# Kernel optimization log

Hardware: AMD Instinct MI355X
Metric: run time of the kernel (lower is better)

The kernel has to match this reference:

```python
import jax, jax.numpy as jnp
import numpy as np

B, F_IN, N_D, N_A, VBS, N_STEPS = 1024, 256, 64, 64, 128, 3
FO = N_D + N_A            # 128
D_CAT = 2 * F_IN          # 512
AD = F_IN                 # attention_dim = 256
GAMMA, EPSILON, BN_EPS = 1.3, 1e-15, 1e-5
SQRT_HALF = 0.7071067811865476


def _bn(x, w, b):
    # full-batch BatchNorm1d (training mode, biased var)
    m = x.mean(0)
    v = x.var(0)
    return (x - m) / jnp.sqrt(v + BN_EPS) * w + b


def _gbn(x, w, b):
    # Ghost BatchNorm: per virtual-batch statistics
    n, f = x.shape
    xr = x.reshape(n // VBS, VBS, f)
    m = xr.mean(1, keepdims=True)
    v = xr.var(1, keepdims=True)
    return (xr - m).reshape(n, f) / jnp.sqrt(v + BN_EPS).repeat(VBS, axis=0).reshape(n, f) * w + b


def _glu(x, fcw, bnw, bnb):
    h = _gbn(x @ fcw.T, bnw, bnb)
    d = h.shape[-1] // 2
    return h[:, :d] * jax.nn.sigmoid(h[:, d:])


def _feat_transformer(x, fc0, bnw0, bnb0, fc1, bnw1, bnb1):
    # independent GLU block, first=True, n_glu_independent=2
    h = _glu(x, fc0, bnw0, bnb0)
    return (h + _glu(h, fc1, bnw1, bnb1)) * SQRT_HALF


def _sparsemax(z):
    f = z.shape[-1]
    zs = -jnp.sort(-z, axis=-1)                      # descending
    k = jnp.arange(1, f + 1, dtype=z.dtype)
    zc = jnp.cumsum(zs, axis=-1)
    support = (1.0 + k * zs) > zc
    kz = jnp.sum(support, axis=-1, keepdims=True)
    tau = (jnp.take_along_axis(zc, kz - 1, axis=-1) - 1.0) / kz.astype(z.dtype)
    return jnp.maximum(z - tau, 0.0)


def _self_attn_1d(x, in_w, in_b, out_w, out_b):
    # nn.MultiheadAttention(embed_dim=1, heads=1) over the feature axis
    q = x * in_w[0] + in_b[0]
    k = x * in_w[1] + in_b[1]
    v = x * in_w[2] + in_b[2]
    attn = jax.nn.softmax(jnp.einsum('bi,bj->bij', q, k), axis=-1)  # scale 1/sqrt(1)
    y = jnp.einsum('bij,bj->bi', attn, v) * out_w + out_b
    return y, attn


def setup_inputs() -> dict:
    key = jax.random.key(0)
    ks = iter(jax.random.split(key, 32))
    s = 0.1
    d = {
        'x': jax.random.normal(next(ks), (B, F_IN), jnp.float32),
        'bemv': jax.random.normal(next(ks), (B, F_IN), jnp.float32),
        'gmat': jax.random.uniform(next(ks), (AD, F_IN), jnp.float32),
        'bn_w': jnp.ones((F_IN,), jnp.float32),
        'bn_b': jnp.zeros((F_IN,), jnp.float32),
        'init_fc0': jax.random.normal(next(ks), (2 * FO, D_CAT), jnp.float32) * s,
        'init_bnw0': jnp.ones((2 * FO,), jnp.float32),
        'init_bnb0': jnp.zeros((2 * FO,), jnp.float32),
        'init_fc1': jax.random.normal(next(ks), (2 * FO, FO), jnp.float32) * s,
        'init_bnw1': jnp.ones((2 * FO,), jnp.float32),
        'init_bnb1': jnp.zeros((2 * FO,), jnp.float32),
        'step_fc0': jax.random.normal(next(ks), (N_STEPS, 2 * FO, D_CAT), jnp.float32) * s,
        'step_bnw0': jnp.ones((N_STEPS, 2 * FO), jnp.float32),
        'step_bnb0': jnp.zeros((N_STEPS, 2 * FO), jnp.float32),
        'step_fc1': jax.random.normal(next(ks), (N_STEPS, 2 * FO, FO), jnp.float32) * s,
        'step_bnw1': jnp.ones((N_STEPS, 2 * FO), jnp.float32),
        'step_bnb1': jnp.zeros((N_STEPS, 2 * FO), jnp.float32),
        'att_fc': jax.random.normal(next(ks), (N_STEPS, AD, N_A), jnp.float32) * s,
        'att_bnw': jnp.ones((N_STEPS, AD), jnp.float32),
        'att_bnb': jnp.zeros((N_STEPS, AD), jnp.float32),
        'sa_in_w': jax.random.normal(next(ks), (N_STEPS, 3), jnp.float32),
        'sa_in_b': jnp.zeros((N_STEPS, 3), jnp.float32),
        'sa_out_w': jax.random.normal(next(ks), (N_STEPS,), jnp.float32),
        'sa_out_b': jnp.zeros((N_STEPS,), jnp.float32),
    }
    return d


def reference(x, bemv, gmat, bn_w, bn_b,
              init_fc0, init_bnw0, init_bnb0, init_fc1, init_bnw1, init_bnb1,
              step_fc0, step_bnw0, step_bnb0, step_fc1, step_bnw1, step_bnb1,
              att_fc, att_bnw, att_bnb,
              sa_in_w, sa_in_b, sa_out_w, sa_out_b):
    prior = jnp.ones((x.shape[0], AD), x.dtype)
    xn = _bn(x, bn_w, bn_b)
    x_cat = jnp.concatenate([xn, bemv], axis=1)
    feat_out = _feat_transformer(x_cat, init_fc0, init_bnw0, init_bnb0,
                                 init_fc1, init_bnw1, init_bnb1)
    att = feat_out[:, N_D:]
    m_loss = jnp.asarray(0.0, x.dtype)
    steps, amaps = [], []
    for s in range(N_STEPS):
        a = _gbn(att @ att_fc[s].T, att_bnw[s], att_bnb[s])
        tab_mask = _sparsemax(a * prior)
        m_loss = m_loss + jnp.mean(jnp.sum(tab_mask * jnp.log(tab_mask + EPSILON), axis=1))
        prior = prior * (GAMMA - tab_mask)
        x_masked = (tab_mask @ gmat) * xn
        x_masked, A = _self_attn_1d(x_masked, sa_in_w[s], sa_in_b[s], sa_out_w[s], sa_out_b[s])
        amaps.append(A)
        feat_out = _feat_transformer(jnp.concatenate([x_masked, bemv], axis=1),
                                     step_fc0[s], step_bnw0[s], step_bnb0[s],
                                     step_fc1[s], step_bnw1[s], step_bnb1[s])
        steps.append(jax.nn.leaky_relu(feat_out[:, :N_D], 0.01))
        att = feat_out[:, N_D:]
    m_loss = m_loss / N_STEPS
    return jnp.stack(steps), m_loss, jnp.stack(amaps)
```

## Files before the change

kernel.cpp:

```cpp
#include <hip/hip_runtime.h>
#include <hip/hip_bf16.h>

#define BATCH 1024
#define F_IN 256
#define N_D 64
#define N_A 64
#define VBS 128
#define N_STEPS 3
#define FO 128
#define D_CAT 512
#define AD 256
#define GAMMA_C 1.3f
#define BN_EPS_C 1e-5f
#define SQRT_HALF_C 0.70710678118654752440f

__device__ __forceinline__ float ldin(const void* p, size_t i, int isbf){
  if (isbf) return __bfloat162float(((const __hip_bfloat16*)p)[i]);
  return ((const float*)p)[i];
}
__device__ __forceinline__ float4 ld4(const void* p, size_t i, int isbf){
  if (!isbf) return *(const float4*)((const float*)p + i);
  const __hip_bfloat16* q = (const __hip_bfloat16*)p + i;
  return make_float4(__bfloat162float(q[0]), __bfloat162float(q[1]),
                     __bfloat162float(q[2]), __bfloat162float(q[3]));
}

__device__ __forceinline__ float wsum(float v){
#pragma unroll
  for (int o = 32; o > 0; o >>= 1) v += __shfl_xor(v, o);
  return v;
}
__device__ __forceinline__ float wmaxr(float v){
#pragma unroll
  for (int o = 32; o > 0; o >>= 1) v = fmaxf(v, __shfl_xor(v, o));
  return v;
}
__device__ __forceinline__ float wminr(float v){
#pragma unroll
  for (int o = 32; o > 0; o >>= 1) v = fminf(v, __shfl_xor(v, o));
  return v;
}
__device__ __forceinline__ float block_sum(float v, float* sb){
  int t = threadIdx.x;
  sb[t] = v; __syncthreads();
#pragma unroll
  for (int s = 128; s > 0; s >>= 1){
    if (t < s) sb[t] += sb[t + s];
    __syncthreads();
  }
  float r = sb[0]; __syncthreads();
  return r;
}

__global__ void detect_k(const unsigned short* __restrict__ u, float* __restrict__ flag){
  __shared__ int cnt;
  if (threadIdx.x == 0) cnt = 0;
  __syncthreads();
  int c = 0;
  for (int j = 0; j < 16; ++j){
    unsigned short v = u[(size_t)(threadIdx.x * 16 + j) * 2];
    int e = (v >> 7) & 0xFF;
    if (e >= 118 && e <= 134) c++;
  }
  atomicAdd(&cnt, c);
  __syncthreads();
  if (threadIdx.x == 0) flag[0] = (cnt > 2048) ? 1.0f : 0.0f;
}

__global__ void bnstats_k(const void* __restrict__ x, float* __restrict__ mean,
                          float* __restrict__ istd, const float* __restrict__ flg){
  __shared__ float sb[256];
  const int isbf = flg[0] != 0.0f;
  int f = blockIdx.x, t = threadIdx.x;
  float s = 0.f, ss = 0.f;
  for (int r = t; r < BATCH; r += 256){
    float v = ldin(x, (size_t)r * F_IN + f, isbf);
    s += v; ss += v * v;
  }
  s  = block_sum(s, sb);
  ss = block_sum(ss, sb);
  if (t == 0){
    float m = s * (1.f / BATCH);
    mean[f] = m;
    istd[f] = rsqrtf(ss * (1.f / BATCH) - m * m + BN_EPS_C);
  }
}

__global__ void xn_k(const void* __restrict__ x, const float* __restrict__ mean,
                     const float* __restrict__ istd, const void* __restrict__ bw,
                     const void* __restrict__ bb, float* __restrict__ xn,
                     const float* __restrict__ flg){
  const int isbf = flg[0] != 0.0f;
  int idx = blockIdx.x * 256 + threadIdx.x;
  int f = idx & (F_IN - 1);
  xn[idx] = (ldin(x, idx, isbf) - mean[f]) * istd[f] * ldin(bw, f, isbf) + ldin(bb, f, isbf);
}

__global__ __launch_bounds__(256)
void gemm_bt_k(const float* __restrict__ A1, const void* __restrict__ A2, int split,
               const void* __restrict__ W, size_t woff, float* __restrict__ C,
               int K, const float* __restrict__ flg){
  __shared__ float As[32][34];
  __shared__ float Ws[32][34];
  const int isbf = flg[0] != 0.0f;
  const int n0 = blockIdx.x * 32, m0 = blockIdx.y * 32;
  const int t = threadIdx.x;
  const int tx = t & 15, ty = t >> 4;
  const int lr = t >> 3, lk = (t & 7) * 4;
  const int nc = K >> 5;
  float a00 = 0.f, a01 = 0.f, a10 = 0.f, a11 = 0.f;

  auto lda = [&](int k0) -> float4 {
    int gk = k0 + lk, gr = m0 + lr;
    if (gk < split) return *(const float4*)(A1 + (size_t)gr * split + gk);
    return ld4(A2, (size_t)gr * (K - split) + (gk - split), isbf);
  };
  auto ldw = [&](int k0) -> float4 {
    return ld4(W, woff + (size_t)(n0 + lr) * K + k0 + lk, isbf);
  };

  float4 ra = lda(0), rw = ldw(0);
  for (int c = 0; c < nc; ++c){
    As[lk+0][lr] = ra.x; As[lk+1][lr] = ra.y; As[lk+2][lr] = ra.z; As[lk+3][lr] = ra.w;
    Ws[lk+0][lr] = rw.x; Ws[lk+1][lr] = rw.y; Ws[lk+2][lr] = rw.z; Ws[lk+3][lr] = rw.w;
    __syncthreads();
    float4 na = ra, nw = rw;
    if (c + 1 < nc){ na = lda((c+1) << 5); nw = ldw((c+1) << 5); }
#pragma unroll
    for (int kk = 0; kk < 32; ++kk){
      float2 av = *(const float2*)&As[kk][ty*2];
      float2 wv = *(const float2*)&Ws[kk][tx*2];
      a00 += av.x * wv.x; a01 += av.x * wv.y;
      a10 += av.y * wv.x; a11 += av.y * wv.y;
    }
    __syncthreads();
    ra = na; rw = nw;
  }
  int r0 = m0 + ty*2, c0 = n0 + tx*2;
  float* Cp = C + (size_t)r0 * 256 + c0;
  Cp[0] = a00; Cp[1] = a01; Cp[256] = a10; Cp[257] = a11;
}

__global__ __launch_bounds__(256)
void gemm_glu_k(const float* __restrict__ H1, const float* __restrict__ saf,
                const float* __restrict__ sbf, const void* __restrict__ W,
                size_t woff, float* __restrict__ C, const float* __restrict__ flg){
  __shared__ float As[32][34];
  __shared__ float Ws[32][34];
  const int isbf = flg[0] != 0.0f;
  const int n0 = blockIdx.x * 32, m0 = blockIdx.y * 32;
  const int t = threadIdx.x;
  const int tx = t & 15, ty = t >> 4;
  const int lr = t >> 3, lk = (t & 7) * 4;
  float a00 = 0.f, a01 = 0.f, a10 = 0.f, a11 = 0.f;

  auto lda = [&](int k0) -> float4 {
    int gk = k0 + lk, gr = m0 + lr, g = gr >> 7;
    float4 h0 = *(const float4*)(H1 + (size_t)gr*256 + gk);
    float4 h1 = *(const float4*)(H1 + (size_t)gr*256 + gk + 128);
    float4 A0 = *(const float4*)(saf + g*256 + gk);
    float4 B0 = *(const float4*)(sbf + g*256 + gk);
    float4 A1 = *(const float4*)(saf + g*256 + gk + 128);
    float4 B1 = *(const float4*)(sbf + g*256 + gk + 128);
    float4 r;
    r.x = (h0.x*A0.x + B0.x) / (1.f + __expf(-(h1.x*A1.x + B1.x)));
    r.y = (h0.y*A0.y + B0.y) / (1.f + __expf(-(h1.y*A1.y + B1.y)));
    r.z = (h0.z*A0.z + B0.z) / (1.f + __expf(-(h1.z*A1.z + B1.z)));
    r.w = (h0.w*A0.w + B0.w) / (1.f + __expf(-(h1.w*A1.w + B1.w)));
    return r;
  };
  auto ldw = [&](int k0) -> float4 {
    return ld4(W, woff + (size_t)(n0 + lr) * 128 + k0 + lk, isbf);
  };

  float4 ra = lda(0), rw = ldw(0);
#pragma unroll 1
  for (int c = 0; c < 4; ++c){
    As[lk+0][lr] = ra.x; As[lk+1][lr] = ra.y; As[lk+2][lr] = ra.z; As[lk+3][lr] = ra.w;
    Ws[lk+0][lr] = rw.x; Ws[lk+1][lr] = rw.y; Ws[lk+2][lr] = rw.z; Ws[lk+3][lr] = rw.w;
    __syncthreads();
    float4 na = ra, nw = rw;
    if (c + 1 < 4){ na = lda((c+1) << 5); nw = ldw((c+1) << 5); }
#pragma unroll
    for (int kk = 0; kk < 32; ++kk){
      float2 av = *(const float2*)&As[kk][ty*2];
      float2 wv = *(const float2*)&Ws[kk][tx*2];
      a00 += av.x * wv.x; a01 += av.x * wv.y;
      a10 += av.y * wv.x; a11 += av.y * wv.y;
    }
    __syncthreads();
    ra = na; rw = nw;
  }
  int r0 = m0 + ty*2, c0 = n0 + tx*2;
  float* Cp = C + (size_t)r0 * 256 + c0;
  Cp[0] = a00; Cp[1] = a01; Cp[256] = a10; Cp[257] = a11;
}

__global__ __launch_bounds__(256)
void gstats_k(const float* __restrict__ H, const void* __restrict__ w,
              const void* __restrict__ b, size_t off, float* __restrict__ sa,
              float* __restrict__ sb, const float* __restrict__ flg){
  __shared__ float ps[8][32], pss[8][32];
  const int isbf = flg[0] != 0.0f;
  int c0 = blockIdx.x * 32, g = blockIdx.y;
  int tx = threadIdx.x & 31, q = threadIdx.x >> 5;
  const float* Hp = H + ((size_t)g*128 + q*16) * 256 + c0 + tx;
  float s = 0.f, ss = 0.f;
#pragma unroll
  for (int i = 0; i < 16; ++i){ float v = Hp[(size_t)i*256]; s += v; ss += v*v; }
  ps[q][tx] = s; pss[q][tx] = ss;
  __syncthreads();
  if (threadIdx.x < 32){
    int t = threadIdx.x, col = c0 + t;
    float S = 0.f, SS = 0.f;
#pragma unroll
    for (int qq = 0; qq < 8; ++qq){ S += ps[qq][t]; SS += pss[qq][t]; }
    float m = S * (1.f/128), is = rsqrtf(SS * (1.f/128) - m*m + BN_EPS_C);
    float wv = ldin(w, off + col, isbf), bv = ldin(b, off + col, isbf);
    float A = is * wv;
    sa[g*256 + col] = A;
    sb[g*256 + col] = bv - m * A;
  }
}

__global__ __launch_bounds__(256)
void spmaxxm_k(const float* __restrict__ H, const float* __restrict__ sa,
               const float* __restrict__ sb, float* __restrict__ prior,
               const float* __restrict__ xn, const void* __restrict__ gmat,
               float* __restrict__ xm, float* __restrict__ lrow,
               int first, const float* __restrict__ flg){
  __shared__ __align__(16) float tabs[4][256];
  __shared__ unsigned int msk[4][2];
  const int isbf = flg[0] != 0.0f;
  int lane = threadIdx.x & 63, wv = threadIdx.x >> 6;
  int b0 = blockIdx.x * 4;
  int b = b0 + wv, g = b >> 7;
  size_t rb = (size_t)b * 256;
  int j0 = lane * 4;
  float4 h4 = *(const float4*)(H + rb + j0);
  float4 A4 = *(const float4*)(sa + (size_t)g*256 + j0);
  float4 B4 = *(const float4*)(sb + (size_t)g*256 + j0);
  float pr[4];
  if (first){ pr[0] = pr[1] = pr[2] = pr[3] = 1.f; }
  else { float4 p4 = *(const float4*)(prior + rb + j0); pr[0]=p4.x; pr[1]=p4.y; pr[2]=p4.z; pr[3]=p4.w; }
  float z[4];
  z[0] = (h4.x*A4.x + B4.x) * pr[0];
  z[1] = (h4.y*A4.y + B4.y) * pr[1];
  z[2] = (h4.z*A4.z + B4.z) * pr[2];
  z[3] = (h4.w*A4.w + B4.w) * pr[3];
  float zm = wmaxr(fmaxf(fmaxf(z[0], z[1]), fmaxf(z[2], z[3])));
  float lo = zm - 1.f, hi = zm;
#pragma unroll 1
  for (int it = 0; it < 30; ++it){
    float mid = 0.5f * (lo + hi);
    float s = 0.f;
#pragma unroll
    for (int e = 0; e < 4; ++e){ float d = z[e] - mid; s += d > 0.f ? d : 0.f; }
    s = wsum(s);
    if (s >= 1.f) lo = mid; else hi = mid;
  }
  float tau = 0.5f * (lo + hi);
  float p[4], ls = 0.f;
#pragma unroll
  for (int e = 0; e < 4; ++e){
    p[e] = z[e] - tau; p[e] = p[e] > 0.f ? p[e] : 0.f;
    ls += p[e] * __logf(p[e] + 1e-15f);
  }
  *(float4*)&tabs[wv][j0] = make_float4(p[0], p[1], p[2], p[3]);
  *(float4*)(prior + rb + j0) = make_float4(pr[0]*(GAMMA_C - p[0]), pr[1]*(GAMMA_C - p[1]),
                                            pr[2]*(GAMMA_C - p[2]), pr[3]*(GAMMA_C - p[3]));
  ls = wsum(ls);
  if (lane == 0) lrow[b] = ls;
  bool nz = (p[0] > 0.f) | (p[1] > 0.f) | (p[2] > 0.f) | (p[3] > 0.f);
  unsigned long long bm = __ballot(nz);
  if (lane == 0){ msk[wv][0] = (unsigned int)bm; msk[wv][1] = (unsigned int)(bm >> 32); }
  __syncthreads();
  int t = threadIdx.x;
  unsigned long long M0 = msk[0][0] | ((unsigned long long)msk[0][1] << 32);
  unsigned long long M1 = msk[1][0] | ((unsigned long long)msk[1][1] << 32);
  unsigned long long M2 = msk[2][0] | ((unsigned long long)msk[2][1] << 32);
  unsigned long long M3 = msk[3][0] | ((unsigned long long)msk[3][1] << 32);
  float a0 = 0.f, a1 = 0.f, a2 = 0.f, a3 = 0.f;
#pragma unroll 1
  for (int c = 0; c < 64; ++c){
    int r0a = (int)((M0 >> c) & 1), r1a = (int)((M1 >> c) & 1);
    int r2a = (int)((M2 >> c) & 1), r3a = (int)((M3 >> c) & 1);
    if (r0a | r1a | r2a | r3a){
      int k = c * 4;
      float g0 = ldin(gmat, (size_t)(k+0)*256 + t, isbf);
      float g1 = ldin(gmat, (size_t)(k+1)*256 + t, isbf);
      float g2 = ldin(gmat, (size_t)(k+2)*256 + t, isbf);
      float g3 = ldin(gmat, (size_t)(k+3)*256 + t, isbf);
      if (r0a){ float4 tv = *(float4*)&tabs[0][k]; a0 += tv.x*g0 + tv.y*g1 + tv.z*g2 + tv.w*g3; }
      if (r1a){ float4 tv = *(float4*)&tabs[1][k]; a1 += tv.x*g0 + tv.y*g1 + tv.z*g2 + tv.w*g3; }
      if (r2a){ float4 tv = *(float4*)&tabs[2][k]; a2 += tv.x*g0 + tv.y*g1 + tv.z*g2 + tv.w*g3; }
      if (r3a){ float4 tv = *(float4*)&tabs[3][k]; a3 += tv.x*g0 + tv.y*g1 + tv.z*g2 + tv.w*g3; }
    }
  }
  xm[(size_t)(b0+0)*256 + t] = a0 * xn[(size_t)(b0+0)*256 + t];
  xm[(size_t)(b0+1)*256 + t] = a1 * xn[(size_t)(b0+1)*256 + t];
  xm[(size_t)(b0+2)*256 + t] = a2 * xn[(size_t)(b0+2)*256 + t];
  xm[(size_t)(b0+3)*256 + t] = a3 * xn[(size_t)(b0+3)*256 + t];
}

__global__ __launch_bounds__(256)
void attn_k(const float* __restrict__ xm, float* __restrict__ y,
            const void* __restrict__ in_w, const void* __restrict__ in_b,
            const void* __restrict__ out_w, const void* __restrict__ out_b,
            int s, float* __restrict__ amap, const float* __restrict__ flg){
  __shared__ __align__(16) float qs[256], ks[256], vs[256], ms[256], rz[256];
  __shared__ float r1[4], r2[4];
  const int isbf = flg[0] != 0.0f;
  int b = blockIdx.x, t = threadIdx.x;
  float w0 = ldin(in_w, s*3+0, isbf), w1 = ldin(in_w, s*3+1, isbf), w2 = ldin(in_w, s*3+2, isbf);
  float b0 = ldin(in_b, s*3+0, isbf), b1 = ldin(in_b, s*3+1, isbf), b2 = ldin(in_b, s*3+2, isbf);
  float ow = ldin(out_w, s, isbf), ob = ldin(out_b, s, isbf);
  float xv = xm[(size_t)b*256 + t];
  float q = xv*w0 + b0, k = xv*w1 + b1, v = xv*w2 + b2;
  qs[t] = q; ks[t] = k; vs[t] = v;
  int lane = t & 63, wv = t >> 6;
  float km = wmaxr(k), kn = wminr(k);
  if (lane == 0){ r1[wv] = km; r2[wv] = kn; }
  __syncthreads();
  float kmax = fmaxf(fmaxf(r1[0], r1[1]), fmaxf(r1[2], r1[3]));
  float kmin = fminf(fminf(r2[0], r2[1]), fminf(r2[2], r2[3]));
  float mi = (q >= 0.f) ? q*kmax : q*kmin;
  float Z = 0.f, Y = 0.f;
#pragma unroll 8
  for (int j = 0; j < 256; j += 4){
    float4 k4 = *(const float4*)&ks[j];
    float4 v4 = *(const float4*)&vs[j];
    float e0 = __expf(q*k4.x - mi), e1 = __expf(q*k4.y - mi);
    float e2 = __expf(q*k4.z - mi), e3 = __expf(q*k4.w - mi);
    Z += (e0 + e1) + (e2 + e3);
    Y += (e0*v4.x + e1*v4.y) + (e2*v4.z + e3*v4.w);
  }
  float rzv = 1.f / Z;
  y[(size_t)b*256 + t] = Y*rzv*ow + ob;
  ms[t] = mi; rz[t] = rzv;
  __syncthreads();
  int c0 = (t & 127) * 2;
  int rh = (t >> 7) * 128;
  float k0 = ks[c0], k1 = ks[c0 + 1];
  size_t base = ((size_t)s*BATCH + b) * 65536 + c0;
#pragma unroll 8
  for (int i = 0; i < 128; i += 4){
    int r = rh + i;
    float4 q4 = *(const float4*)&qs[r];
    float4 m4 = *(const float4*)&ms[r];
    float4 s4 = *(const float4*)&rz[r];
    float e00 = __expf(q4.x*k0 - m4.x) * s4.x, e01 = __expf(q4.x*k1 - m4.x) * s4.x;
    float e10 = __expf(q4.y*k0 - m4.y) * s4.y, e11 = __expf(q4.y*k1 - m4.y) * s4.y;
    float e20 = __expf(q4.z*k0 - m4.z) * s4.z, e21 = __expf(q4.z*k1 - m4.z) * s4.z;
    float e30 = __expf(q4.w*k0 - m4.w) * s4.w, e31 = __expf(q4.w*k1 - m4.w) * s4.w;
    *(float2*)(amap + base + (size_t)(r+0)*256) = make_float2(e00, e01);
    *(float2*)(amap + base + (size_t)(r+1)*256) = make_float2(e10, e11);
    *(float2*)(amap + base + (size_t)(r+2)*256) = make_float2(e20, e21);
    *(float2*)(amap + base + (size_t)(r+3)*256) = make_float2(e30, e31);
  }
}

__global__ __launch_bounds__(256)
void combine_k(const float* __restrict__ H1, const float* __restrict__ sa0,
               const float* __restrict__ sb0, const float* __restrict__ H2,
               const float* __restrict__ sa1, const float* __restrict__ sb1,
               float* __restrict__ att, float* __restrict__ steps_out){
  int r = blockIdx.x * 2 + (threadIdx.x >> 7);
  int j = threadIdx.x & 127;
  int g = r >> 7;
  float h0 = H1[(size_t)r*256 + j],  h1 = H1[(size_t)r*256 + j + 128];
  float n0 = h0 * sa0[g*256 + j]     + sb0[g*256 + j];
  float n1 = h1 * sa0[g*256 + j+128] + sb0[g*256 + j+128];
  float g0 = n0 / (1.f + __expf(-n1));
  float h2 = H2[(size_t)r*256 + j],  h3 = H2[(size_t)r*256 + j + 128];
  float m0 = h2 * sa1[g*256 + j]     + sb1[g*256 + j];
  float m1 = h3 * sa1[g*256 + j+128] + sb1[g*256 + j+128];
  float g1 = m0 / (1.f + __expf(-m1));
  float f = (g0 + g1) * SQRT_HALF_C;
  if (j < 64){
    if (steps_out) steps_out[(size_t)r*64 + j] = f > 0.f ? f : 0.01f*f;
  } else {
    att[(size_t)r*64 + (j - 64)] = f;
  }
}

__global__ void mloss_k(const float* __restrict__ lrow, float* __restrict__ outp){
  __shared__ float sb[256];
  int t = threadIdx.x;
  float s = 0.f;
  for (int i = t; i < N_STEPS*BATCH; i += 256) s += lrow[i];
  s = block_sum(s, sb);
  if (t == 0) outp[0] = s * (1.f/(N_STEPS*(float)BATCH));
}

extern "C" void kernel_launch(void* const* d_in, const int* in_sizes, int n_in,
                              void* d_out, int out_size, void* d_ws, size_t ws_size,
                              hipStream_t stream){
  const void* x         = d_in[0];
  const void* bemv      = d_in[1];
  const void* gmat      = d_in[2];
  const void* bn_w      = d_in[3];
  const void* bn_b      = d_in[4];
  const void* init_fc0  = d_in[5];
  const void* init_bnw0 = d_in[6];
  const void* init_bnb0 = d_in[7];
  const void* init_fc1  = d_in[8];
  const void* init_bnw1 = d_in[9];
  const void* init_bnb1 = d_in[10];
  const void* step_fc0  = d_in[11];
  const void* step_bnw0 = d_in[12];
  const void* step_bnb0 = d_in[13];
  const void* step_fc1  = d_in[14];
  const void* step_bnw1 = d_in[15];
  const void* step_bnb1 = d_in[16];
  const void* att_fc    = d_in[17];
  const void* att_bnw   = d_in[18];
  const void* att_bnb   = d_in[19];
  const void* sa_in_w   = d_in[20];
  const void* sa_in_b   = d_in[21];
  const void* sa_out_w  = d_in[22];
  const void* sa_out_b  = d_in[23];

  float* out       = (float*)d_out;
  float* steps_out = out;
  float* mloss_out = out + (size_t)N_STEPS*BATCH*N_D;
  float* amaps     = mloss_out + 1;

  float* w     = (float*)d_ws;
  float* flag  = w;
  float* mean  = w + 16;
  float* istd  = w + 272;
  float* lrow  = w + 528;
  float* sa0   = w + 4096;
  float* sb0   = sa0 + 2048;
  float* sa1   = sb0 + 2048;
  float* sb1   = sa1 + 2048;
  float* saA   = sb1 + 2048;
  float* sbA   = saA + 2048;
  float* xn    = w + 16384;
  float* H1    = xn   + 262144;
  float* H2    = H1   + 262144;
  float* att   = H2   + 262144;
  float* xm    = att  + 65536;
  float* prior = xm   + 262144;
  float* y     = prior + 262144;

  dim3 gemmGrid(8, 32);
  dim3 gstGrid(8, 8);

  detect_k<<<1, 256, 0, stream>>>((const unsigned short*)x, flag);
  bnstats_k<<<256, 256, 0, stream>>>(x, mean, istd, flag);
  xn_k<<<1024, 256, 0, stream>>>(x, mean, istd, bn_w, bn_b, xn, flag);

  gemm_bt_k<<<gemmGrid, 256, 0, stream>>>(xn, bemv, 256, init_fc0, 0, H1, 512, flag);
  gstats_k<<<gstGrid, 256, 0, stream>>>(H1, init_bnw0, init_bnb0, 0, sa0, sb0, flag);
  gemm_glu_k<<<gemmGrid, 256, 0, stream>>>(H1, sa0, sb0, init_fc1, 0, H2, flag);
  gstats_k<<<gstGrid, 256, 0, stream>>>(H2, init_bnw1, init_bnb1, 0, sa1, sb1, flag);
  combine_k<<<512, 256, 0, stream>>>(H1, sa0, sb0, H2, sa1, sb1, att, nullptr);

  for (int s = 0; s < N_STEPS; ++s){
    gemm_bt_k<<<gemmGrid, 256, 0, stream>>>(att, nullptr, 64, att_fc, (size_t)s*AD*N_A, H1, 64, flag);
    gstats_k<<<gstGrid, 256, 0, stream>>>(H1, att_bnw, att_bnb, (size_t)s*256, saA, sbA, flag);
    spmaxxm_k<<<256, 256, 0, stream>>>(H1, saA, sbA, prior, xn, gmat, xm, lrow + s*1024, s == 0, flag);
    attn_k<<<1024, 256, 0, stream>>>(xm, y, sa_in_w, sa_in_b, sa_out_w, sa_out_b, s, amaps, flag);
    gemm_bt_k<<<gemmGrid, 256, 0, stream>>>(y, bemv, 256, step_fc0, (size_t)s*256*512, H1, 512, flag);
    gstats_k<<<gstGrid, 256, 0, stream>>>(H1, step_bnw0, step_bnb0, (size_t)s*256, sa0, sb0, flag);
    gemm_glu_k<<<gemmGrid, 256, 0, stream>>>(H1, sa0, sb0, step_fc1, (size_t)s*256*128, H2, flag);
    gstats_k<<<gstGrid, 256, 0, stream>>>(H2, step_bnw1, step_bnb1, (size_t)s*256, sa1, sb1, flag);
    combine_k<<<512, 256, 0, stream>>>(H1, sa0, sb0, H2, sa1, sb1, att,
                                       steps_out + (size_t)s*BATCH*N_D);
  }
  mloss_k<<<1, 256, 0, stream>>>(lrow, mloss_out);
}
```

Measured before the change: 440.4 us.

## Defer attention-map writes into spare blocks of later kernels; fuse GBN stats into consumers

The attention kernel now stores only per-row q, k, max and 1/Z to a staging buffer instead of writing the full 256x256 attention map per row. Extra "drain" blocks are appended to later kernels (the GEMMs, GLU-GEMM, combine, sparsemax and the next step's attention), and they expand those rows into the amap output. This overlaps the large amap store traffic with compute-bound kernels. Separately, the ghost-batchnorm stats kernels are removed and each consumer block recomputes the group statistics itself. That cuts launches but adds redundant column reductions and a staging buffer round trip.

Result: no change. 443.0 us (+0.6%).

```diff
diff --git a/kernel.cpp b/kernel.cpp
--- a/kernel.cpp
+++ b/kernel.cpp
@@ -2,17 +2,11 @@
 #include <hip/hip_bf16.h>
 
 #define BATCH 1024
-#define F_IN 256
-#define N_D 64
-#define N_A 64
-#define VBS 128
 #define N_STEPS 3
-#define FO 128
-#define D_CAT 512
-#define AD 256
 #define GAMMA_C 1.3f
 #define BN_EPS_C 1e-5f
 #define SQRT_HALF_C 0.70710678118654752440f
+#define ST_STRIDE 786432
 
 __device__ __forceinline__ float ldin(const void* p, size_t i, int isbf){
   if (isbf) return __bfloat162float(((const __hip_bfloat16*)p)[i]);
@@ -52,6 +46,39 @@
   return r;
 }
 
+__device__ __forceinline__ void drain_rows(const float* __restrict__ st,
+                                           float* __restrict__ amap,
+                                           int s, int b, int t){
+  __shared__ __align__(16) float sh[768];
+  const float* qS = st;
+  const float* kS = st + ST_STRIDE;
+  const float* mS = st + 2*ST_STRIDE;
+  const float* rS = st + 3*ST_STRIDE;
+  size_t sb = ((size_t)s*BATCH + b)*256;
+  sh[t]       = qS[sb + t];
+  sh[256 + t] = mS[sb + t];
+  sh[512 + t] = rS[sb + t];
+  __syncthreads();
+  int c0 = (t & 127)*2, rh = (t >> 7)*128;
+  float k0 = kS[sb + c0], k1 = kS[sb + c0 + 1];
+  size_t base = ((size_t)s*BATCH + b)*65536 + c0;
+#pragma unroll 8
+  for (int i = 0; i < 128; i += 4){
+    int r = rh + i;
+    float4 q4 = *(const float4*)&sh[r];
+    float4 m4 = *(const float4*)&sh[256 + r];
+    float4 s4 = *(const float4*)&sh[512 + r];
+    float e00 = __expf(q4.x*k0 - m4.x) * s4.x, e01 = __expf(q4.x*k1 - m4.x) * s4.x;
+    float e10 = __expf(q4.y*k0 - m4.y) * s4.y, e11 = __expf(q4.y*k1 - m4.y) * s4.y;
+    float e20 = __expf(q4.z*k0 - m4.z) * s4.z, e21 = __expf(q4.z*k1 - m4.z) * s4.z;
+    float e30 = __expf(q4.w*k0 - m4.w) * s4.w, e31 = __expf(q4.w*k1 - m4.w) * s4.w;
+    *(float2*)(amap + base + (size_t)(r+0)*256) = make_float2(e00, e01);
+    *(float2*)(amap + base + (size_t)(r+1)*256) = make_float2(e10, e11);
+    *(float2*)(amap + base + (size_t)(r+2)*256) = make_float2(e20, e21);
+    *(float2*)(amap + base + (size_t)(r+3)*256) = make_float2(e30, e31);
+  }
+}
+
 __global__ void detect_k(const unsigned short* __restrict__ u, float* __restrict__ flag){
   __shared__ int cnt;
   if (threadIdx.x == 0) cnt = 0;
@@ -74,7 +101,7 @@
   int f = blockIdx.x, t = threadIdx.x;
   float s = 0.f, ss = 0.f;
   for (int r = t; r < BATCH; r += 256){
-    float v = ldin(x, (size_t)r * F_IN + f, isbf);
+    float v = ldin(x, (size_t)r * 256 + f, isbf);
     s += v; ss += v * v;
   }
   s  = block_sum(s, sb);
@@ -92,19 +119,21 @@
                      const float* __restrict__ flg){
   const int isbf = flg[0] != 0.0f;
   int idx = blockIdx.x * 256 + threadIdx.x;
-  int f = idx & (F_IN - 1);
+  int f = idx & 255;
   xn[idx] = (ldin(x, idx, isbf) - mean[f]) * istd[f] * ldin(bw, f, isbf) + ldin(bb, f, isbf);
 }
 
 __global__ __launch_bounds__(256)
 void gemm_bt_k(const float* __restrict__ A1, const void* __restrict__ A2, int split,
-               const void* __restrict__ W, size_t woff, float* __restrict__ C,
-               int K, const float* __restrict__ flg){
+               const void* __restrict__ W, size_t woff, float* __restrict__ C, int K,
+               const float* __restrict__ st, float* __restrict__ amap, int dS, int dR0,
+               const float* __restrict__ flg){
+  int bid = blockIdx.x, t = threadIdx.x;
+  if (bid >= 256){ drain_rows(st, amap, dS, dR0 + bid - 256, t); return; }
   __shared__ float As[32][34];
   __shared__ float Ws[32][34];
   const int isbf = flg[0] != 0.0f;
-  const int n0 = blockIdx.x * 32, m0 = blockIdx.y * 32;
-  const int t = threadIdx.x;
+  const int n0 = (bid & 7) * 32, m0 = (bid >> 3) * 32;
   const int tx = t & 15, ty = t >> 4;
   const int lr = t >> 3, lk = (t & 7) * 4;
   const int nc = K >> 5;
@@ -142,31 +171,48 @@
 }
 
 __global__ __launch_bounds__(256)
-void gemm_glu_k(const float* __restrict__ H1, const float* __restrict__ saf,
-                const float* __restrict__ sbf, const void* __restrict__ W,
-                size_t woff, float* __restrict__ C, const float* __restrict__ flg){
+void glugemm_k(const float* __restrict__ H1, const void* __restrict__ gw,
+               const void* __restrict__ gb, size_t goff,
+               const void* __restrict__ W, size_t woff, float* __restrict__ C,
+               const float* __restrict__ st, float* __restrict__ amap, int dS, int dR0,
+               const float* __restrict__ flg){
+  int bid = blockIdx.x, t = threadIdx.x;
+  if (bid >= 256){ drain_rows(st, amap, dS, dR0 + bid - 256, t); return; }
+  __shared__ __align__(16) float sA[256], sB[256];
   __shared__ float As[32][34];
   __shared__ float Ws[32][34];
   const int isbf = flg[0] != 0.0f;
-  const int n0 = blockIdx.x * 32, m0 = blockIdx.y * 32;
-  const int t = threadIdx.x;
+  const int n0 = (bid & 7) * 32, m0 = (bid >> 3) * 32;
+  const int g = bid >> 5;
+  {
+    const float* Hp = H1 + (size_t)g*32768 + t;
+    float s = 0.f, ss = 0.f;
+#pragma unroll 8
+    for (int i = 0; i < 128; ++i){ float v = Hp[(size_t)i*256]; s += v; ss += v*v; }
+    float m = s * (1.f/128), is = rsqrtf(ss * (1.f/128) - m*m + BN_EPS_C);
+    float wv = ldin(gw, goff + t, isbf), bv = ldin(gb, goff + t, isbf);
+    float A = is * wv;
+    sA[t] = A; sB[t] = bv - m*A;
+  }
+  __syncthreads();
   const int tx = t & 15, ty = t >> 4;
   const int lr = t >> 3, lk = (t & 7) * 4;
   float a00 = 0.f, a01 = 0.f, a10 = 0.f, a11 = 0.f;
 
   auto lda = [&](int k0) -> float4 {
-    int gk = k0 + lk, gr = m0 + lr, g = gr >> 7;
-    float4 h0 = *(const float4*)(H1 + (size_t)gr*256 + gk);
-    float4 h1 = *(const float4*)(H1 + (size_t)gr*256 + gk + 128);
-    float4 A0 = *(const float4*)(saf + g*256 + gk);
-    float4 B0 = *(const float4*)(sbf + g*256 + gk);
-    float4 A1 = *(const float4*)(saf + g*256 + gk + 128);
-    float4 B1 = *(const float4*)(sbf + g*256 + gk + 128);
+    int gk = k0 + lk, gr = m0 + lr;
+    const float* h = H1 + (size_t)gr*256;
+    float4 h0 = *(const float4*)(h + gk);
+    float4 h1 = *(const float4*)(h + gk + 128);
+    float4 A0 = *(const float4*)(sA + gk);
+    float4 B0 = *(const float4*)(sB + gk);
+    float4 A1 = *(const float4*)(sA + gk + 128);
+    float4 B1 = *(const float4*)(sB + gk + 128);
     float4 r;
-    r.x = (h0.x*A0.x + B0.x) / (1.f + __expf(-(h1.x*A1.x + B1.x)));
-    r.y = (h0.y*A0.y + B0.y) / (1.f + __expf(-(h1.y*A1.y + B1.y)));
-    r.z = (h0.z*A0.z + B0.z) / (1.f + __expf(-(h1.z*A1.z + B1.z)));
-    r.w = (h0.w*A0.w + B0.w) / (1.f + __expf(-(h1.w*A1.w + B1.w)));
+    r.x = (h0.x*A0.x+B0.x) / (1.f + __expf(-(h1.x*A1.x+B1.x)));
+    r.y = (h0.y*A0.y+B0.y) / (1.f + __expf(-(h1.y*A1.y+B1.y)));
+    r.z = (h0.z*A0.z+B0.z) / (1.f + __expf(-(h1.z*A1.z+B1.z)));
+    r.w = (h0.w*A0.w+B0.w) / (1.f + __expf(-(h1.w*A1.w+B1.w)));
     return r;
   };
   auto ldw = [&](int k0) -> float4 {
@@ -197,49 +243,38 @@
 }
 
 __global__ __launch_bounds__(256)
-void gstats_k(const float* __restrict__ H, const void* __restrict__ w,
-              const void* __restrict__ b, size_t off, float* __restrict__ sa,
-              float* __restrict__ sb, const float* __restrict__ flg){
-  __shared__ float ps[8][32], pss[8][32];
-  const int isbf = flg[0] != 0.0f;
-  int c0 = blockIdx.x * 32, g = blockIdx.y;
-  int tx = threadIdx.x & 31, q = threadIdx.x >> 5;
-  const float* Hp = H + ((size_t)g*128 + q*16) * 256 + c0 + tx;
-  float s = 0.f, ss = 0.f;
-#pragma unroll
-  for (int i = 0; i < 16; ++i){ float v = Hp[(size_t)i*256]; s += v; ss += v*v; }
-  ps[q][tx] = s; pss[q][tx] = ss;
-  __syncthreads();
-  if (threadIdx.x < 32){
-    int t = threadIdx.x, col = c0 + t;
-    float S = 0.f, SS = 0.f;
-#pragma unroll
-    for (int qq = 0; qq < 8; ++qq){ S += ps[qq][t]; SS += pss[qq][t]; }
-    float m = S * (1.f/128), is = rsqrtf(SS * (1.f/128) - m*m + BN_EPS_C);
-    float wv = ldin(w, off + col, isbf), bv = ldin(b, off + col, isbf);
-    float A = is * wv;
-    sa[g*256 + col] = A;
-    sb[g*256 + col] = bv - m * A;
-  }
-}
-
-__global__ __launch_bounds__(256)
-void spmaxxm_k(const float* __restrict__ H, const float* __restrict__ sa,
-               const float* __restrict__ sb, float* __restrict__ prior,
-               const float* __restrict__ xn, const void* __restrict__ gmat,
-               float* __restrict__ xm, float* __restrict__ lrow,
-               int first, const float* __restrict__ flg){
+void spmax_k(const float* __restrict__ Ha, const void* __restrict__ gw,
+             const void* __restrict__ gb, size_t goff, float* __restrict__ prior,
+             const float* __restrict__ xn, const void* __restrict__ gmat,
+             float* __restrict__ xm, float* __restrict__ lrow, int first,
+             const float* __restrict__ st, float* __restrict__ amap, int dS, int dR0,
+             const float* __restrict__ flg){
+  int bid = blockIdx.x, t = threadIdx.x;
+  if (bid >= 256){ drain_rows(st, amap, dS, dR0 + bid - 256, t); return; }
+  __shared__ __align__(16) float sAA[256], sBA[256];
   __shared__ __align__(16) float tabs[4][256];
   __shared__ unsigned int msk[4][2];
   const int isbf = flg[0] != 0.0f;
-  int lane = threadIdx.x & 63, wv = threadIdx.x >> 6;
-  int b0 = blockIdx.x * 4;
-  int b = b0 + wv, g = b >> 7;
+  const int g = bid >> 5;
+  {
+    const float* Hp = Ha + (size_t)g*32768 + t;
+    float s = 0.f, ss = 0.f;
+#pragma unroll 8
+    for (int i = 0; i < 128; ++i){ float v = Hp[(size_t)i*256]; s += v; ss += v*v; }
+    float m = s * (1.f/128), is = rsqrtf(ss * (1.f/128) - m*m + BN_EPS_C);
+    float wv = ldin(gw, goff + t, isbf), bv = ldin(gb, goff + t, isbf);
+    float A = is * wv;
+    sAA[t] = A; sBA[t] = bv - m*A;
+  }
+  __syncthreads();
+  int lane = t & 63, wv = t >> 6;
+  int b0 = bid * 4;
+  int b = b0 + wv;
   size_t rb = (size_t)b * 256;
   int j0 = lane * 4;
-  float4 h4 = *(const float4*)(H + rb + j0);
-  float4 A4 = *(const float4*)(sa + (size_t)g*256 + j0);
-  float4 B4 = *(const float4*)(sb + (size_t)g*256 + j0);
+  float4 h4 = *(const float4*)(Ha + rb + j0);
+  float4 A4 = *(const float4*)(sAA + j0);
+  float4 B4 = *(const float4*)(sBA + j0);
   float pr[4];
   if (first){ pr[0] = pr[1] = pr[2] = pr[3] = 1.f; }
   else { float4 p4 = *(const float4*)(prior + rb + j0); pr[0]=p4.x; pr[1]=p4.y; pr[2]=p4.z; pr[3]=p4.w; }
@@ -253,11 +288,11 @@
 #pragma unroll 1
   for (int it = 0; it < 30; ++it){
     float mid = 0.5f * (lo + hi);
-    float s = 0.f;
-#pragma unroll
-    for (int e = 0; e < 4; ++e){ float d = z[e] - mid; s += d > 0.f ? d : 0.f; }
-    s = wsum(s);
-    if (s >= 1.f) lo = mid; else hi = mid;
+    float sv = 0.f;
+#pragma unroll
+    for (int e = 0; e < 4; ++e){ float d = z[e] - mid; sv += d > 0.f ? d : 0.f; }
+    sv = wsum(sv);
+    if (sv >= 1.f) lo = mid; else hi = mid;
   }
   float tau = 0.5f * (lo + hi);
   float p[4], ls = 0.f;
@@ -267,15 +302,14 @@
     ls += p[e] * __logf(p[e] + 1e-15f);
   }
   *(float4*)&tabs[wv][j0] = make_float4(p[0], p[1], p[2], p[3]);
-  *(float4*)(prior + rb + j0) = make_float4(pr[0]*(GAMMA_C - p[0]), pr[1]*(GAMMA_C - p[1]),
-                                            pr[2]*(GAMMA_C - p[2]), pr[3]*(GAMMA_C - p[3]));
+  *(float4*)(prior + rb + j0) = make_float4(pr[0]*(GAMMA_C-p[0]), pr[1]*(GAMMA_C-p[1]),
+                                            pr[2]*(GAMMA_C-p[2]), pr[3]*(GAMMA_C-p[3]));
   ls = wsum(ls);
   if (lane == 0) lrow[b] = ls;
   bool nz = (p[0] > 0.f) | (p[1] > 0.f) | (p[2] > 0.f) | (p[3] > 0.f);
   unsigned long long bm = __ballot(nz);
   if (lane == 0){ msk[wv][0] = (unsigned int)bm; msk[wv][1] = (unsigned int)(bm >> 32); }
   __syncthreads();
-  int t = threadIdx.x;
   unsigned long long M0 = msk[0][0] | ((unsigned long long)msk[0][1] << 32);
   unsigned long long M1 = msk[1][0] | ((unsigned long long)msk[1][1] << 32);
   unsigned long long M2 = msk[2][0] | ((unsigned long long)msk[2][1] << 32);
@@ -304,20 +338,23 @@
 }
 
 __global__ __launch_bounds__(256)
-void attn_k(const float* __restrict__ xm, float* __restrict__ y,
-            const void* __restrict__ in_w, const void* __restrict__ in_b,
-            const void* __restrict__ out_w, const void* __restrict__ out_b,
-            int s, float* __restrict__ amap, const float* __restrict__ flg){
-  __shared__ __align__(16) float qs[256], ks[256], vs[256], ms[256], rz[256];
+void attnA_k(const float* __restrict__ xm, float* __restrict__ y,
+             const void* __restrict__ siw, const void* __restrict__ sib,
+             const void* __restrict__ sow, const void* __restrict__ sob,
+             int s, float* __restrict__ st, float* __restrict__ amap, int dS, int dR0,
+             const float* __restrict__ flg){
+  int bid = blockIdx.x, t = threadIdx.x;
+  if (bid >= 1024){ drain_rows(st, amap, dS, dR0 + bid - 1024, t); return; }
+  __shared__ __align__(16) float ks[256], vs[256];
   __shared__ float r1[4], r2[4];
   const int isbf = flg[0] != 0.0f;
-  int b = blockIdx.x, t = threadIdx.x;
-  float w0 = ldin(in_w, s*3+0, isbf), w1 = ldin(in_w, s*3+1, isbf), w2 = ldin(in_w, s*3+2, isbf);
-  float b0 = ldin(in_b, s*3+0, isbf), b1 = ldin(in_b, s*3+1, isbf), b2 = ldin(in_b, s*3+2, isbf);
-  float ow = ldin(out_w, s, isbf), ob = ldin(out_b, s, isbf);
+  int b = bid;
+  float w0 = ldin(siw, s*3+0, isbf), w1 = ldin(siw, s*3+1, isbf), w2 = ldin(siw, s*3+2, isbf);
+  float b0 = ldin(sib, s*3+0, isbf), b1 = ldin(sib, s*3+1, isbf), b2 = ldin(sib, s*3+2, isbf);
+  float ow = ldin(sow, s, isbf), ob = ldin(sob, s, isbf);
   float xv = xm[(size_t)b*256 + t];
   float q = xv*w0 + b0, k = xv*w1 + b1, v = xv*w2 + b2;
-  qs[t] = q; ks[t] = k; vs[t] = v;
+  ks[t] = k; vs[t] = v;
   int lane = t & 63, wv = t >> 6;
   float km = wmaxr(k), kn = wminr(k);
   if (lane == 0){ r1[wv] = km; r2[wv] = kn; }
@@ -335,53 +372,68 @@
     Z += (e0 + e1) + (e2 + e3);
     Y += (e0*v4.x + e1*v4.y) + (e2*v4.z + e3*v4.w);
   }
-  float rzv = 1.f / Z;
-  y[(size_t)b*256 + t] = Y*rzv*ow + ob;
-  ms[t] = mi; rz[t] = rzv;
-  __syncthreads();
-  int c0 = (t & 127) * 2;
-  int rh = (t >> 7) * 128;
-  float k0 = ks[c0], k1 = ks[c0 + 1];
-  size_t base = ((size_t)s*BATCH + b) * 65536 + c0;
+  float rz = 1.f / Z;
+  y[(size_t)b*256 + t] = Y*rz*ow + ob;
+  size_t sb = ((size_t)s*BATCH + b)*256 + t;
+  st[sb]               = q;
+  st[ST_STRIDE + sb]   = k;
+  st[2*ST_STRIDE + sb] = mi;
+  st[3*ST_STRIDE + sb] = rz;
+}
+
+__global__ __launch_bounds__(256)
+void comb_k(const float* __restrict__ H1, const void* __restrict__ pw0,
+            const void* __restrict__ pb0, size_t off0,
+            const float* __restrict__ H2, const void* __restrict__ pw1,
+            const void* __restrict__ pb1, size_t off1,
+            float* __restrict__ att, float* __restrict__ steps,
+            const float* __restrict__ st, float* __restrict__ amap, int dS, int dR0,
+            const float* __restrict__ flg){
+  int bid = blockIdx.x, t = threadIdx.x;
+  if (bid >= 512){ drain_rows(st, amap, dS, dR0 + bid - 512, t); return; }
+  __shared__ float sA0[256], sB0[256], sA1[256], sB1[256];
+  const int isbf = flg[0] != 0.0f;
+  const int g = bid >> 6;
+  {
+    const float* Hp = H1 + (size_t)g*32768 + t;
+    float s = 0.f, ss = 0.f;
 #pragma unroll 8
-  for (int i = 0; i < 128; i += 4){
-    int r = rh + i;
-    float4 q4 = *(const float4*)&qs[r];
-    float4 m4 = *(const float4*)&ms[r];
-    float4 s4 = *(const float4*)&rz[r];
-    float e00 = __expf(q4.x*k0 - m4.x) * s4.x, e01 = __expf(q4.x*k1 - m4.x) * s4.x;
-    float e10 = __expf(q4.y*k0 - m4.y) * s4.y, e11 = __expf(q4.y*k1 - m4.y) * s4.y;
-    float e20 = __expf(q4.z*k0 - m4.z) * s4.z, e21 = __expf(q4.z*k1 - m4.z) * s4.z;
-    float e30 = __expf(q4.w*k0 - m4.w) * s4.w, e31 = __expf(q4.w*k1 - m4.w) * s4.w;
-    *(float2*)(amap + base + (size_t)(r+0)*256) = make_float2(e00, e01);
-    *(float2*)(amap + base + (size_t)(r+1)*256) = make_float2(e10, e11);
-    *(float2*)(amap + base + (size_t)(r+2)*256) = make_float2(e20, e21);
-    *(float2*)(amap + base + (size_t)(r+3)*256) = make_float2(e30, e31);
-  }
-}
-
-__global__ __launch_bounds__(256)
-void combine_k(const float* __restrict__ H1, const float* __restrict__ sa0,
-               const float* __restrict__ sb0, const float* __restrict__ H2,
-               const float* __restrict__ sa1, const float* __restrict__ sb1,
-               float* __restrict__ att, float* __restrict__ steps_out){
-  int r = blockIdx.x * 2 + (threadIdx.x >> 7);
-  int j = threadIdx.x & 127;
-  int g = r >> 7;
-  float h0 = H1[(size_t)r*256 + j],  h1 = H1[(size_t)r*256 + j + 128];
-  float n0 = h0 * sa0[g*256 + j]     + sb0[g*256 + j];
-  float n1 = h1 * sa0[g*256 + j+128] + sb0[g*256 + j+128];
-  float g0 = n0 / (1.f + __expf(-n1));
-  float h2 = H2[(size_t)r*256 + j],  h3 = H2[(size_t)r*256 + j + 128];
-  float m0 = h2 * sa1[g*256 + j]     + sb1[g*256 + j];
-  float m1 = h3 * sa1[g*256 + j+128] + sb1[g*256 + j+128];
-  float g1 = m0 / (1.f + __expf(-m1));
+    for (int i = 0; i < 128; ++i){ float v = Hp[(size_t)i*256]; s += v; ss += v*v; }
+    float m = s * (1.f/128), is = rsqrtf(ss * (1.f/128) - m*m + BN_EPS_C);
+    float wv = ldin(pw0, off0 + t, isbf), bv = ldin(pb0, off0 + t, isbf);
+    float A = is * wv;
+    sA0[t] = A; sB0[t] = bv - m*A;
+  }
+  {
+    const float* Hp = H2 + (size_t)g*32768 + t;
+    float s = 0.f, ss = 0.f;
+#pragma unroll 8
+    for (int i = 0; i < 128; ++i){ float v = Hp[(size_t)i*256]; s += v; ss += v*v; }
+    float m = s * (1.f/128), is = rsqrtf(ss * (1.f/128) - m*m + BN_EPS_C);
+    float wv = ldin(pw1, off1 + t, isbf), bv = ldin(pb1, off1 + t, isbf);
+    float A = is * wv;
+    sA1[t] = A; sB1[t] = bv - m*A;
+  }
+  __syncthreads();
+  int r = bid*2 + (t >> 7), j = t & 127;
+  float h0 = H1[(size_t)r*256 + j], h1 = H1[(size_t)r*256 + j + 128];
+  float u0 = h0 * sA0[j]     + sB0[j];
+  float u1 = h1 * sA0[j+128] + sB0[j+128];
+  float g0 = u0 / (1.f + __expf(-u1));
+  float v0 = H2[(size_t)r*256 + j]     * sA1[j]     + sB1[j];
+  float v1 = H2[(size_t)r*256 + j+128] * sA1[j+128] + sB1[j+128];
+  float g1 = v0 / (1.f + __expf(-v1));
   float f = (g0 + g1) * SQRT_HALF_C;
   if (j < 64){
-    if (steps_out) steps_out[(size_t)r*64 + j] = f > 0.f ? f : 0.01f*f;
+    if (steps) steps[(size_t)r*64 + j] = f > 0.f ? f : 0.01f*f;
   } else {
     att[(size_t)r*64 + (j - 64)] = f;
   }
+}
+
+__global__ __launch_bounds__(256)
+void drain_k(const float* __restrict__ st, float* __restrict__ amap, int s, int row0){
+  drain_rows(st, amap, s, row0 + blockIdx.x, threadIdx.x);
 }
 
 __global__ void mloss_k(const float* __restrict__ lrow, float* __restrict__ outp){
@@ -423,52 +475,49 @@
 
   float* out       = (float*)d_out;
   float* steps_out = out;
-  float* mloss_out = out + (size_t)N_STEPS*BATCH*N_D;
-  float* amaps     = mloss_out + 1;
+  float* mloss_out = out + 196608;
+  float* amaps     = out + 196609;
 
   float* w     = (float*)d_ws;
   float* flag  = w;
   float* mean  = w + 16;
   float* istd  = w + 272;
   float* lrow  = w + 528;
-  float* sa0   = w + 4096;
-  float* sb0   = sa0 + 2048;
-  float* sa1   = sb0 + 2048;
-  float* sb1   = sa1 + 2048;
-  float* saA   = sb1 + 2048;
-  float* sbA   = saA + 2048;
-  float* xn    = w + 16384;
-  float* H1    = xn   + 262144;
-  float* H2    = H1   + 262144;
-  float* att   = H2   + 262144;
-  float* xm    = att  + 65536;
-  float* prior = xm   + 262144;
+  float* xn    = w + 4096;
+  float* H1    = xn + 262144;
+  float* H2    = H1 + 262144;
+  float* att   = H2 + 262144;
+  float* xm    = att + 65536;
+  float* prior = xm + 262144;
   float* y     = prior + 262144;
-
-  dim3 gemmGrid(8, 32);
-  dim3 gstGrid(8, 8);
+  float* st    = y + 262144;
 
   detect_k<<<1, 256, 0, stream>>>((const unsigned short*)x, flag);
   bnstats_k<<<256, 256, 0, stream>>>(x, mean, istd, flag);
   xn_k<<<1024, 256, 0, stream>>>(x, mean, istd, bn_w, bn_b, xn, flag);
 
-  gemm_bt_k<<<gemmGrid, 256, 0, stream>>>(xn, bemv, 256, init_fc0, 0, H1, 512, flag);
-  gstats_k<<<gstGrid, 256, 0, stream>>>(H1, init_bnw0, init_bnb0, 0, sa0, sb0, flag);
-  gemm_glu_k<<<gemmGrid, 256, 0, stream>>>(H1, sa0, sb0, init_fc1, 0, H2, flag);
-  gstats_k<<<gstGrid, 256, 0, stream>>>(H2, init_bnw1, init_bnb1, 0, sa1, sb1, flag);
-  combine_k<<<512, 256, 0, stream>>>(H1, sa0, sb0, H2, sa1, sb1, att, nullptr);
+  gemm_bt_k<<<256, 256, 0, stream>>>(xn, bemv, 256, init_fc0, 0, H1, 512, st, amaps, 0, 0, flag);
+  glugemm_k<<<256, 256, 0, stream>>>(H1, init_bnw0, init_bnb0, 0, init_fc1, 0, H2, st, amaps, 0, 0, flag);
+  comb_k<<<512, 256, 0, stream>>>(H1, init_bnw0, init_bnb0, 0, H2, init_bnw1, init_bnb1, 0,
+                                  att, nullptr, st, amaps, 0, 0, flag);
 
   for (int s = 0; s < N_STEPS; ++s){
-    gemm_bt_k<<<gemmGrid, 256, 0, stream>>>(att, nullptr, 64, att_fc, (size_t)s*AD*N_A, H1, 64, flag);
-    gstats_k<<<gstGrid, 256, 0, stream>>>(H1, att_bnw, att_bnb, (size_t)s*256, saA, sbA, flag);
-    spmaxxm_k<<<256, 256, 0, stream>>>(H1, saA, sbA, prior, xn, gmat, xm, lrow + s*1024, s == 0, flag);
-    attn_k<<<1024, 256, 0, stream>>>(xm, y, sa_in_w, sa_in_b, sa_out_w, sa_out_b, s, amaps, flag);
-    gemm_bt_k<<<gemmGrid, 256, 0, stream>>>(y, bemv, 256, step_fc0, (size_t)s*256*512, H1, 512, flag);
-    gstats_k<<<gstGrid, 256, 0, stream>>>(H1, step_bnw0, step_bnb0, (size_t)s*256, sa0, sb0, flag);
-    gemm_glu_k<<<gemmGrid, 256, 0, stream>>>(H1, sa0, sb0, step_fc1, (size_t)s*256*128, H2, flag);
-    gstats_k<<<gstGrid, 256, 0, stream>>>(H2, step_bnw1, step_bnb1, (size_t)s*256, sa1, sb1, flag);
-    combine_k<<<512, 256, 0, stream>>>(H1, sa0, sb0, H2, sa1, sb1, att,
-                                       steps_out + (size_t)s*BATCH*N_D);
-  }
+    int pd = s - 1;
+    int dn = (pd >= 0) ? 160 : 0;
+    gemm_bt_k<<<256 + dn, 256, 0, stream>>>(att, nullptr, 64, att_fc, (size_t)s*16384, H1, 64,
+                                            st, amaps, pd, 544, flag);
+    spmax_k<<<256 + dn, 256, 0, stream>>>(H1, att_bnw, att_bnb, (size_t)s*256, prior, xn, gmat,
+                                          xm, lrow + s*1024, s == 0, st, amaps, pd, 704, flag);
+    attnA_k<<<1024 + dn, 256, 0, stream>>>(xm, y, sa_in_w, sa_in_b, sa_out_w, sa_out_b, s,
+                                           st, amaps, pd, 864, flag);
+    gemm_bt_k<<<256 + 224, 256, 0, stream>>>(y, bemv, 256, step_fc0, (size_t)s*131072, H1, 512,
+                                             st, amaps, s, 0, flag);
+    glugemm_k<<<256 + 160, 256, 0, stream>>>(H1, step_bnw0, step_bnb0, (size_t)s*256,
+                                             step_fc1, (size_t)s*32768, H2, st, amaps, s, 224, flag);
+    comb_k<<<512 + 160, 256, 0, stream>>>(H1, step_bnw0, step_bnb0, (size_t)s*256,
+                                          H2, step_bnw1, step_bnb1, (size_t)s*256,
+                                          att, steps_out + (size_t)s*65536, st, amaps, s, 384, flag);
+  }
+  drain_k<<<480, 256, 0, stream>>>(st, amaps, 2, 544);
   mloss_k<<<1, 256, 0, stream>>>(lrow, mloss_out);
 }
```
